# Kernel tuning notes

Measured on AMD Instinct MI355X. Metric: run time of the kernel, lower is better.

## Reference

```python
import jax, jax.numpy as jnp
import numpy as np

NUM_HEADS = 16
HEAD_DIM = 64  # hidden_size 1024 / 16 heads


def setup_inputs() -> dict:
    key = jax.random.key(0)
    ks = jax.random.split(key, 4)
    B, S, H = 2, 2048, 1024
    scale = 1.0 / np.sqrt(H)
    return {
        "hidden_states": jax.random.normal(ks[0], (B, S, H), dtype=jnp.float32),
        "attention_mask": jnp.zeros((B, 1, 1, S), dtype=jnp.float32),
        "Wq": jax.random.normal(ks[1], (H, H), dtype=jnp.float32) * scale,
        "bq": jnp.zeros((H,), dtype=jnp.float32),
        "Wk": jax.random.normal(ks[2], (H, H), dtype=jnp.float32) * scale,
        "bk": jnp.zeros((H,), dtype=jnp.float32),
        "Wv": jax.random.normal(ks[3], (H, H), dtype=jnp.float32) * scale,
        "bv": jnp.zeros((H,), dtype=jnp.float32),
    }


def reference(hidden_states, attention_mask, Wq, bq, Wk, bk, Wv, bv):
    B, S, H = hidden_states.shape
    h, d = NUM_HEADS, HEAD_DIM

    def heads(x):  # [B,S,H] -> [B,h,S,d]
        return x.reshape(B, S, h, d).transpose(0, 2, 1, 3)

    q = heads(hidden_states @ Wq + bq)
    k = heads(hidden_states @ Wk + bk)
    v = heads(hidden_states @ Wv + bv)

    # [B,h,S,S] scores, scaled then additive-masked (HF BERT semantics)
    scores = jnp.einsum("bhqd,bhkd->bhqk", q, k) / jnp.sqrt(jnp.float32(d))
    scores = scores + attention_mask
    probs = jax.nn.softmax(scores, axis=-1)  # dropout p=0 -> identity

    ctx = jnp.einsum("bhqk,bhkd->bhqd", probs, v)
    ctx = ctx.transpose(0, 2, 1, 3).reshape(B, S, H)
    return ctx
```

## Files before the change

kernel.cpp:

```cpp
#include <hip/hip_runtime.h>
#include <hip/hip_bf16.h>


#define SEQ   2048
#define HID   1024
#define NHEAD 16
#define HD    64
#define SD    ((size_t)SEQ * HD)

typedef __bf16 bf16x8 __attribute__((ext_vector_type(8)));
typedef float  f32x4  __attribute__((ext_vector_type(4)));

#define L2E 1.4426950408889634f
#define SOFT_OFF 16.0f

__device__ __forceinline__ unsigned short f2b(float f) {
    unsigned int x = __float_as_uint(f);
    x += 0x7FFFu + ((x >> 16) & 1u);
    return (unsigned short)(x >> 16);
}

__device__ __forceinline__ void gload16(const unsigned short* g,
                                        unsigned short* l) {
    __builtin_amdgcn_global_load_lds(
        (const __attribute__((address_space(1))) unsigned int*)g,
        (__attribute__((address_space(3))) unsigned int*)l, 16, 0, 0);
}

__global__ __launch_bounds__(256) void cvt_x_k(const float* __restrict__ X,
                                               unsigned short* __restrict__ Xb)
{
    const size_t i = ((size_t)blockIdx.x * 256 + threadIdx.x) * 4;
    const float4 v = *(const float4*)(X + i);
    ushort4 o;
    o.x = f2b(v.x); o.y = f2b(v.y); o.z = f2b(v.z); o.w = f2b(v.w);
    *(ushort4*)(Xb + i) = o;
}

__global__ __launch_bounds__(256) void cvt_w_k(
    const float* __restrict__ Wq, const float* __restrict__ Wk,
    const float* __restrict__ Wv, unsigned short* __restrict__ Wtb)
{
    __shared__ __align__(16) unsigned short T[64][68];
    const int z = blockIdx.z;
    const float* __restrict__ W = (z == 0) ? Wq : (z == 1) ? Wk : Wv;
    const int k0 = blockIdx.x * 64, n0 = blockIdx.y * 64;
    const int tid = threadIdx.x;
    #pragma unroll
    for (int it = 0; it < 16; ++it) {
        const int idx = 256 * it + tid;
        const int r = idx >> 6, c = idx & 63;
        T[c][r] = f2b(W[(size_t)(k0 + r) * HID + n0 + c]);
    }
    __syncthreads();
    unsigned short* dst = Wtb + (size_t)z * HID * HID;
    #pragma unroll
    for (int it = 0; it < 4; ++it) {
        const int idx = 256 * it + tid;
        const int n = idx >> 4, c4 = (idx & 15) * 4;
        *(ushort4*)(dst + (size_t)(n0 + n) * HID + k0 + c4) = *(ushort4*)&T[n][c4];
    }
}

__device__ __forceinline__ void gemm_epilogue(
    f32x4 acc[4][4], const float* __restrict__ Bp,
    unsigned short* __restrict__ scratch, unsigned short (*Et)[68],
    int z, int m0, int n0, int wr, int wc, int ln, int quad)
{
    const int b = m0 >> 11;
    const int srow0 = (m0 + wr) & (SEQ - 1);
    const int head = (n0 + wc) >> 6;
    __syncthreads();

    if (z == 2) {
        #pragma unroll
        for (int half = 0; half < 2; ++half) {
            #pragma unroll
            for (int nt2 = 0; nt2 < 2; ++nt2) {
                const int nt = half * 2 + nt2;
                const float bias = Bp[n0 + wc + nt * 16 + ln];
                #pragma unroll
                for (int mt = 0; mt < 4; ++mt) {
                    ushort4 o;
                    o.x = f2b(acc[mt][nt][0] + bias);
                    o.y = f2b(acc[mt][nt][1] + bias);
                    o.z = f2b(acc[mt][nt][2] + bias);
                    o.w = f2b(acc[mt][nt][3] + bias);
                    *(ushort4*)&Et[nt2 * 16 + ln][mt * 16 + quad * 4] = o;
                }
            }
            __syncthreads();
            #pragma unroll
            for (int it = 0; it < 8; ++it) {
                const int d = it * 4 + quad, s4 = ln * 4;
                *(ushort4*)(scratch +
                    ((size_t)(64 + b * NHEAD + head) * HD + half * 32 + d) * SEQ
                    + srow0 + s4) = *(const ushort4*)&Et[d][s4];
            }
            __syncthreads();
        }
    } else {
        #pragma unroll
        for (int half = 0; half < 2; ++half) {
            #pragma unroll
            for (int mt2 = 0; mt2 < 2; ++mt2) {
                const int mt = half * 2 + mt2;
                #pragma unroll
                for (int nt = 0; nt < 4; ++nt) {
                    const float bias = Bp[n0 + wc + nt * 16 + ln];
                    #pragma unroll
                    for (int r = 0; r < 4; ++r)
                        Et[mt2 * 16 + quad * 4 + r][nt * 16 + ln] =
                            f2b(acc[mt][nt][r] + bias);
                }
            }
            __syncthreads();
            #pragma unroll
            for (int it = 0; it < 8; ++it) {
                const int r = it * 4 + quad, c4 = ln * 4;
                *(ushort4*)(scratch +
                    ((size_t)(z * 32 + b * NHEAD + head) * SEQ + srow0
                     + half * 32 + r) * HD + c4) = *(const ushort4*)&Et[r][c4];
            }
            __syncthreads();
        }
    }
}

__global__ __launch_bounds__(256) void qkv_gemm_bf16(
    const unsigned short* __restrict__ Xb, const unsigned short* __restrict__ Wtb,
    const float* __restrict__ bq, const float* __restrict__ bk,
    const float* __restrict__ bv, unsigned short* __restrict__ scratch)
{
    __shared__ __align__(16) unsigned short pool[2][2][128][32];

    const int z = blockIdx.z;
    const float* __restrict__ Bp = (z == 0) ? bq : (z == 1) ? bk : bv;
    const unsigned short* __restrict__ Wz = Wtb + (size_t)z * HID * HID;

    const int tid = threadIdx.x, w = tid >> 6, lane = tid & 63;
    const int ln = lane & 15, quad = lane >> 4;
    const int wr = (w >> 1) * 64, wc = (w & 1) * 64;
    const int m0 = blockIdx.x * 128, n0 = blockIdx.y * 128;

    const int L0 = w * 128 + lane;
    const int r0 = L0 >> 2,        c0 = (L0 & 3) * 8;
    const int r1 = (L0 + 64) >> 2, c1 = ((L0 + 64) & 3) * 8;

    f32x4 acc[4][4];
    #pragma unroll
    for (int i = 0; i < 4; ++i)
        #pragma unroll
        for (int j = 0; j < 4; ++j) acc[i][j] = (f32x4){0.f, 0.f, 0.f, 0.f};

    {
        unsigned short* lx = &pool[0][0][0][0] + (size_t)(w * 128) * 8;
        unsigned short* lw = &pool[0][1][0][0] + (size_t)(w * 128) * 8;
        gload16(Xb + (size_t)(m0 + r0) * HID + c0, lx);
        gload16(Xb + (size_t)(m0 + r1) * HID + c1, lx + 64 * 8);
        gload16(Wz + (size_t)(n0 + r0) * HID + c0, lw);
        gload16(Wz + (size_t)(n0 + r1) * HID + c1, lw + 64 * 8);
    }

    int cur = 0;
    for (int k0 = 0; k0 < HID; k0 += 32) {
        __syncthreads();
        if (k0 + 32 < HID) {
            const int kn = k0 + 32, nxt = cur ^ 1;
            unsigned short* lx = &pool[nxt][0][0][0] + (size_t)(w * 128) * 8;
            unsigned short* lw = &pool[nxt][1][0][0] + (size_t)(w * 128) * 8;
            gload16(Xb + (size_t)(m0 + r0) * HID + kn + c0, lx);
            gload16(Xb + (size_t)(m0 + r1) * HID + kn + c1, lx + 64 * 8);
            gload16(Wz + (size_t)(n0 + r0) * HID + kn + c0, lw);
            gload16(Wz + (size_t)(n0 + r1) * HID + kn + c1, lw + 64 * 8);
        }

        bf16x8 am[4], bn[4];
        #pragma unroll
        for (int t = 0; t < 4; ++t) {
            am[t] = *(const bf16x8*)&pool[cur][0][wr + t * 16 + ln][quad * 8];
            bn[t] = *(const bf16x8*)&pool[cur][1][wc + t * 16 + ln][quad * 8];
        }
        #pragma unroll
        for (int mt = 0; mt < 4; ++mt)
            #pragma unroll
            for (int nt = 0; nt < 4; ++nt)
                acc[mt][nt] = __builtin_amdgcn_mfma_f32_16x16x32_bf16(
                    am[mt], bn[nt], acc[mt][nt], 0, 0, 0);
        cur ^= 1;
    }
    unsigned short (*Et)[68] =
        (unsigned short (*)[68])((unsigned char*)pool + (size_t)w * 4352);
    gemm_epilogue(acc, Bp, scratch, Et, z, m0, n0, wr, wc, ln, quad);
}

__global__ __launch_bounds__(256) void qkv_gemm_fp32(
    const float* __restrict__ X,
    const float* __restrict__ Wq, const float* __restrict__ bq,
    const float* __restrict__ Wk, const float* __restrict__ bk,
    const float* __restrict__ Wv, const float* __restrict__ bv,
    unsigned short* __restrict__ scratch)
{
    __shared__ __align__(16) unsigned char pool[20480];
    unsigned short (*Xs)[40] = (unsigned short (*)[40])pool;
    unsigned short (*Wt)[40] = (unsigned short (*)[40])(pool + 10240);

    const int z = blockIdx.z;
    const float* __restrict__ W  = (z == 0) ? Wq : (z == 1) ? Wk : Wv;
    const float* __restrict__ Bp = (z == 0) ? bq : (z == 1) ? bk : bv;

    const int tid = threadIdx.x, w = tid >> 6, lane = tid & 63;
    const int ln = lane & 15, quad = lane >> 4;
    const int wr = (w >> 1) * 64, wc = (w & 1) * 64;
    const int m0 = blockIdx.x * 128, n0 = blockIdx.y * 128;

    const int xr = tid >> 3, xc = (tid & 7) * 4;
    const int wkr = tid >> 5, wnc = (tid & 31) * 4;

    f32x4 acc[4][4];
    #pragma unroll
    for (int i = 0; i < 4; ++i)
        #pragma unroll
        for (int j = 0; j < 4; ++j) acc[i][j] = (f32x4){0.f, 0.f, 0.f, 0.f};

    for (int k0 = 0; k0 < HID; k0 += 32) {
        __syncthreads();
        #pragma unroll
        for (int it = 0; it < 4; ++it) {
            const int r = xr + 32 * it;
            const float4 xv = *(const float4*)(X + (size_t)(m0 + r) * HID + k0 + xc);
            ushort4 xb;
            xb.x = f2b(xv.x); xb.y = f2b(xv.y); xb.z = f2b(xv.z); xb.w = f2b(xv.w);
            *(ushort4*)&Xs[r][xc] = xb;
            const int kr = wkr + 8 * it;
            const float4 wv = *(const float4*)(W + (size_t)(k0 + kr) * HID + n0 + wnc);
            Wt[wnc + 0][kr] = f2b(wv.x);
            Wt[wnc + 1][kr] = f2b(wv.y);
            Wt[wnc + 2][kr] = f2b(wv.z);
            Wt[wnc + 3][kr] = f2b(wv.w);
        }
        __syncthreads();
        bf16x8 am[4], bn[4];
        #pragma unroll
        for (int t = 0; t < 4; ++t) {
            am[t] = *(const bf16x8*)&Xs[wr + t * 16 + ln][quad * 8];
            bn[t] = *(const bf16x8*)&Wt[wc + t * 16 + ln][quad * 8];
        }
        #pragma unroll
        for (int mt = 0; mt < 4; ++mt)
            #pragma unroll
            for (int nt = 0; nt < 4; ++nt)
                acc[mt][nt] = __builtin_amdgcn_mfma_f32_16x16x32_bf16(
                    am[mt], bn[nt], acc[mt][nt], 0, 0, 0);
    }
    unsigned short (*Et)[68] = (unsigned short (*)[68])(pool + (size_t)w * 4352);
    gemm_epilogue(acc, Bp, scratch, Et, z, m0, n0, wr, wc, ln, quad);
}

__global__ __launch_bounds__(256) void attn_mfma(
    const unsigned short* __restrict__ scratch,
    const float* __restrict__ mask,
    float* __restrict__ out)
{
    __shared__ __align__(16) unsigned char smem[46080];
    unsigned short (*Ks)[64][72] = (unsigned short (*)[64][72])smem;
    unsigned short (*Vt)[64][72] = (unsigned short (*)[64][72])(smem + 18432);
    unsigned short (*Ps)[72]     = (unsigned short (*)[72])(smem + 36864);
    float (*Obuf)[68] = (float (*)[68])smem;

    const int orig = blockIdx.x;
    const int wg = ((orig & 7) << 7) + (orig >> 3);
    const int qt = wg & 31;
    const int bh = wg >> 5;
    const int b = bh >> 4, head = bh & 15;

    const unsigned short* __restrict__ Qp  = scratch + (size_t)bh * SD;
    const unsigned short* __restrict__ Kp  = scratch + (size_t)(32 + bh) * SD;
    const unsigned short* __restrict__ Vtp = scratch + (size_t)(64 + bh) * SD;
    const float* __restrict__ maskp = mask + b * SEQ;

    const int tid = threadIdx.x, w = tid >> 6, lane = tid & 63;
    const int ln = lane & 15, quad = lane >> 4;

    const int qrow = qt * 64 + w * 16 + ln;
    const bf16x8 qb0 = *(const bf16x8*)(Qp + (size_t)qrow * HD + quad * 8);
    const bf16x8 qb1 = *(const bf16x8*)(Qp + (size_t)qrow * HD + 32 + quad * 8);

    f32x4 O[4];
    #pragma unroll
    for (int t = 0; t < 4; ++t) O[t] = (f32x4){0.f, 0.f, 0.f, 0.f};
    float lr = 0.0f;

    const int sr8 = tid >> 3, sc8 = (tid & 7) * 8;

    {
        uint4 a = *(const uint4*)(Kp + (size_t)sr8 * HD + sc8);
        uint4 c = *(const uint4*)(Kp + (size_t)(sr8 + 32) * HD + sc8);
        uint4 d = *(const uint4*)(Vtp + (size_t)sr8 * SEQ + sc8);
        uint4 e = *(const uint4*)(Vtp + (size_t)(sr8 + 32) * SEQ + sc8);
        *(uint4*)&Ks[0][sr8][sc8]      = a;
        *(uint4*)&Ks[0][sr8 + 32][sc8] = c;
        *(uint4*)&Vt[0][sr8][sc8]      = d;
        *(uint4*)&Vt[0][sr8 + 32][sc8] = e;
    }
    uint4 kg0 = *(const uint4*)(Kp + (size_t)(64 + sr8) * HD + sc8);
    uint4 kg1 = *(const uint4*)(Kp + (size_t)(64 + sr8 + 32) * HD + sc8);
    uint4 vg0 = *(const uint4*)(Vtp + (size_t)sr8 * SEQ + 64 + sc8);
    uint4 vg1 = *(const uint4*)(Vtp + (size_t)(sr8 + 32) * SEQ + 64 + sc8);
    __syncthreads();

    for (int kt = 0; kt < 32; ++kt) {
        const int cur = kt & 1;
        if (kt < 31) {
            *(uint4*)&Ks[cur ^ 1][sr8][sc8]      = kg0;
            *(uint4*)&Ks[cur ^ 1][sr8 + 32][sc8] = kg1;
            *(uint4*)&Vt[cur ^ 1][sr8][sc8]      = vg0;
            *(uint4*)&Vt[cur ^ 1][sr8 + 32][sc8] = vg1;
        }
        if (kt < 30) {
            const int kn = kt + 2;
            kg0 = *(const uint4*)(Kp + (size_t)(kn * 64 + sr8) * HD + sc8);
            kg1 = *(const uint4*)(Kp + (size_t)(kn * 64 + sr8 + 32) * HD + sc8);
            vg0 = *(const uint4*)(Vtp + (size_t)sr8 * SEQ + kn * 64 + sc8);
            vg1 = *(const uint4*)(Vtp + (size_t)(sr8 + 32) * SEQ + kn * 64 + sc8);
        }

        f32x4 s[4];
        #pragma unroll
        for (int t = 0; t < 4; ++t) {
            const bf16x8 ka0 = *(const bf16x8*)&Ks[cur][t * 16 + ln][quad * 8];
            const bf16x8 ka1 = *(const bf16x8*)&Ks[cur][t * 16 + ln][32 + quad * 8];
            f32x4 a = (f32x4){0.f, 0.f, 0.f, 0.f};
            a = __builtin_amdgcn_mfma_f32_16x16x32_bf16(ka0, qb0, a, 0, 0, 0);
            a = __builtin_amdgcn_mfma_f32_16x16x32_bf16(ka1, qb1, a, 0, 0, 0);
            s[t] = a;
        }

        const float c = 0.125f * L2E;
        #pragma unroll
        for (int t = 0; t < 4; ++t) {
            const float4 mk4 = *(const float4*)(maskp + kt * 64 + t * 16 + quad * 4);
            const float b0 = fmaf(mk4.x, L2E, -SOFT_OFF);
            const float b1 = fmaf(mk4.y, L2E, -SOFT_OFF);
            const float b2 = fmaf(mk4.z, L2E, -SOFT_OFF);
            const float b3 = fmaf(mk4.w, L2E, -SOFT_OFF);
            const float p0 = exp2f(fmaf(s[t][0], c, b0));
            const float p1 = exp2f(fmaf(s[t][1], c, b1));
            const float p2 = exp2f(fmaf(s[t][2], c, b2));
            const float p3 = exp2f(fmaf(s[t][3], c, b3));
            lr += (p0 + p1) + (p2 + p3);
            unsigned int w0, w1;
            asm("v_cvt_pk_bf16_f32 %0, %1, %2" : "=v"(w0) : "v"(p0), "v"(p1));
            asm("v_cvt_pk_bf16_f32 %0, %1, %2" : "=v"(w1) : "v"(p2), "v"(p3));
            uint2 pw; pw.x = w0; pw.y = w1;
            *(uint2*)&Ps[w * 16 + ln][t * 16 + quad * 4] = pw;
        }

        const bf16x8 pb0 = *(const bf16x8*)&Ps[w * 16 + ln][quad * 8];
        const bf16x8 pb1 = *(const bf16x8*)&Ps[w * 16 + ln][32 + quad * 8];
        #pragma unroll
        for (int t = 0; t < 4; ++t) {
            const bf16x8 va0 = *(const bf16x8*)&Vt[cur][t * 16 + ln][quad * 8];
            const bf16x8 va1 = *(const bf16x8*)&Vt[cur][t * 16 + ln][32 + quad * 8];
            O[t] = __builtin_amdgcn_mfma_f32_16x16x32_bf16(va0, pb0, O[t], 0, 0, 0);
            O[t] = __builtin_amdgcn_mfma_f32_16x16x32_bf16(va1, pb1, O[t], 0, 0, 0);
        }

        __syncthreads();
    }

    lr += __shfl_xor(lr, 16);
    lr += __shfl_xor(lr, 32);

    const float inv = 1.0f / lr;
    #pragma unroll
    for (int t = 0; t < 4; ++t) {
        float4 o4;
        o4.x = O[t][0] * inv; o4.y = O[t][1] * inv;
        o4.z = O[t][2] * inv; o4.w = O[t][3] * inv;
        *(float4*)&Obuf[w * 16 + ln][t * 16 + quad * 4] = o4;
    }
    __syncthreads();
    #pragma unroll
    for (int it = 0; it < 4; ++it) {
        const int r = (tid >> 4) + 16 * it, c4 = (tid & 15) * 4;
        *(float4*)(out + ((size_t)b * SEQ + qt * 64 + r) * HID + head * HD + c4)
            = *(const float4*)&Obuf[r][c4];
    }
}

extern "C" void kernel_launch(void* const* d_in, const int* in_sizes, int n_in,
                              void* d_out, int out_size, void* d_ws, size_t ws_size,
                              hipStream_t stream) {
    const float* X    = (const float*)d_in[0];
    const float* mask = (const float*)d_in[1];
    const float* Wq   = (const float*)d_in[2];
    const float* bq   = (const float*)d_in[3];
    const float* Wk   = (const float*)d_in[4];
    const float* bk   = (const float*)d_in[5];
    const float* Wv   = (const float*)d_in[6];
    const float* bv   = (const float*)d_in[7];

    unsigned short* scratch = (unsigned short*)d_ws;
    float* out = (float*)d_out;

    const bool big = (ws_size >= (40ull << 20));
    if (big) {
        unsigned short* Xb  = scratch + 96 * SD;
        unsigned short* Wtb = Xb + (size_t)2 * SEQ * HID;
        cvt_x_k<<<4096, 256, 0, stream>>>(X, Xb);
        cvt_w_k<<<dim3(16, 16, 3), 256, 0, stream>>>(Wq, Wk, Wv, Wtb);
        qkv_gemm_bf16<<<dim3(32, 8, 3), 256, 0, stream>>>(
            Xb, Wtb, bq, bk, bv, scratch);
    } else {
        qkv_gemm_fp32<<<dim3(32, 8, 3), 256, 0, stream>>>(
            X, Wq, bq, Wk, bk, Wv, bv, scratch);
    }
    attn_mfma<<<1024, 256, 0, stream>>>(scratch, mask, out);
}
```

Baseline: 199.9 us.

## Load K and V fragments directly from global memory instead of LDS staging

The attention kernel no longer stages K and V tiles into double-buffered shared memory. Each wave now reads its MFMA operand fragments straight from global memory (L2-cached), which removes the per-iteration __syncthreads and shrinks LDS use to hold only the P and output buffers. The intent is to cut synchronisation and LDS traffic and to raise occupancy. The cost is that each of the four waves loads the same K/V data separately, which quadruples global/L2 traffic, and the explicit register prefetch of the next tile is lost.

```diff
diff --git a/kernel.cpp b/kernel.cpp
--- a/kernel.cpp
+++ b/kernel.cpp
@@ -262,10 +262,8 @@
     const float* __restrict__ mask,
     float* __restrict__ out)
 {
-    __shared__ __align__(16) unsigned char smem[46080];
-    unsigned short (*Ks)[64][72] = (unsigned short (*)[64][72])smem;
-    unsigned short (*Vt)[64][72] = (unsigned short (*)[64][72])(smem + 18432);
-    unsigned short (*Ps)[72]     = (unsigned short (*)[72])(smem + 36864);
+    __shared__ __align__(16) unsigned char smem[17408];
+    unsigned short (*Ps)[72] = (unsigned short (*)[72])smem;
     float (*Obuf)[68] = (float (*)[68])smem;
 
     const int orig = blockIdx.x;
@@ -291,52 +289,32 @@
     for (int t = 0; t < 4; ++t) O[t] = (f32x4){0.f, 0.f, 0.f, 0.f};
     float lr = 0.0f;
 
-    const int sr8 = tid >> 3, sc8 = (tid & 7) * 8;
-
-    {
-        uint4 a = *(const uint4*)(Kp + (size_t)sr8 * HD + sc8);
-        uint4 c = *(const uint4*)(Kp + (size_t)(sr8 + 32) * HD + sc8);
-        uint4 d = *(const uint4*)(Vtp + (size_t)sr8 * SEQ + sc8);
-        uint4 e = *(const uint4*)(Vtp + (size_t)(sr8 + 32) * SEQ + sc8);
-        *(uint4*)&Ks[0][sr8][sc8]      = a;
-        *(uint4*)&Ks[0][sr8 + 32][sc8] = c;
-        *(uint4*)&Vt[0][sr8][sc8]      = d;
-        *(uint4*)&Vt[0][sr8 + 32][sc8] = e;
-    }
-    uint4 kg0 = *(const uint4*)(Kp + (size_t)(64 + sr8) * HD + sc8);
-    uint4 kg1 = *(const uint4*)(Kp + (size_t)(64 + sr8 + 32) * HD + sc8);
-    uint4 vg0 = *(const uint4*)(Vtp + (size_t)sr8 * SEQ + 64 + sc8);
-    uint4 vg1 = *(const uint4*)(Vtp + (size_t)(sr8 + 32) * SEQ + 64 + sc8);
-    __syncthreads();
+    const float cc = 0.125f * L2E;
 
     for (int kt = 0; kt < 32; ++kt) {
-        const int cur = kt & 1;
-        if (kt < 31) {
-            *(uint4*)&Ks[cur ^ 1][sr8][sc8]      = kg0;
-            *(uint4*)&Ks[cur ^ 1][sr8 + 32][sc8] = kg1;
-            *(uint4*)&Vt[cur ^ 1][sr8][sc8]      = vg0;
-            *(uint4*)&Vt[cur ^ 1][sr8 + 32][sc8] = vg1;
-        }
-        if (kt < 30) {
-            const int kn = kt + 2;
-            kg0 = *(const uint4*)(Kp + (size_t)(kn * 64 + sr8) * HD + sc8);
-            kg1 = *(const uint4*)(Kp + (size_t)(kn * 64 + sr8 + 32) * HD + sc8);
-            vg0 = *(const uint4*)(Vtp + (size_t)sr8 * SEQ + kn * 64 + sc8);
-            vg1 = *(const uint4*)(Vtp + (size_t)(sr8 + 32) * SEQ + kn * 64 + sc8);
+        const unsigned short* kb = Kp + (size_t)kt * 64 * HD;
+        const unsigned short* vb = Vtp + (size_t)kt * 64;
+        bf16x8 kf0[4], kf1[4], vf0[4], vf1[4];
+        #pragma unroll
+        for (int t = 0; t < 4; ++t) {
+            kf0[t] = *(const bf16x8*)(kb + (size_t)(t * 16 + ln) * HD + quad * 8);
+            kf1[t] = *(const bf16x8*)(kb + (size_t)(t * 16 + ln) * HD + 32 + quad * 8);
+        }
+        #pragma unroll
+        for (int t = 0; t < 4; ++t) {
+            vf0[t] = *(const bf16x8*)(vb + (size_t)(t * 16 + ln) * SEQ + quad * 8);
+            vf1[t] = *(const bf16x8*)(vb + (size_t)(t * 16 + ln) * SEQ + 32 + quad * 8);
         }
 
         f32x4 s[4];
         #pragma unroll
         for (int t = 0; t < 4; ++t) {
-            const bf16x8 ka0 = *(const bf16x8*)&Ks[cur][t * 16 + ln][quad * 8];
-            const bf16x8 ka1 = *(const bf16x8*)&Ks[cur][t * 16 + ln][32 + quad * 8];
             f32x4 a = (f32x4){0.f, 0.f, 0.f, 0.f};
-            a = __builtin_amdgcn_mfma_f32_16x16x32_bf16(ka0, qb0, a, 0, 0, 0);
-            a = __builtin_amdgcn_mfma_f32_16x16x32_bf16(ka1, qb1, a, 0, 0, 0);
+            a = __builtin_amdgcn_mfma_f32_16x16x32_bf16(kf0[t], qb0, a, 0, 0, 0);
+            a = __builtin_amdgcn_mfma_f32_16x16x32_bf16(kf1[t], qb1, a, 0, 0, 0);
             s[t] = a;
         }
 
-        const float c = 0.125f * L2E;
         #pragma unroll
         for (int t = 0; t < 4; ++t) {
             const float4 mk4 = *(const float4*)(maskp + kt * 64 + t * 16 + quad * 4);
@@ -344,10 +322,10 @@
             const float b1 = fmaf(mk4.y, L2E, -SOFT_OFF);
             const float b2 = fmaf(mk4.z, L2E, -SOFT_OFF);
             const float b3 = fmaf(mk4.w, L2E, -SOFT_OFF);
-            const float p0 = exp2f(fmaf(s[t][0], c, b0));
-            const float p1 = exp2f(fmaf(s[t][1], c, b1));
-            const float p2 = exp2f(fmaf(s[t][2], c, b2));
-            const float p3 = exp2f(fmaf(s[t][3], c, b3));
+            const float p0 = exp2f(fmaf(s[t][0], cc, b0));
+            const float p1 = exp2f(fmaf(s[t][1], cc, b1));
+            const float p2 = exp2f(fmaf(s[t][2], cc, b2));
+            const float p3 = exp2f(fmaf(s[t][3], cc, b3));
             lr += (p0 + p1) + (p2 + p3);
             unsigned int w0, w1;
             asm("v_cvt_pk_bf16_f32 %0, %1, %2" : "=v"(w0) : "v"(p0), "v"(p1));
@@ -360,18 +338,15 @@
         const bf16x8 pb1 = *(const bf16x8*)&Ps[w * 16 + ln][32 + quad * 8];
         #pragma unroll
         for (int t = 0; t < 4; ++t) {
-            const bf16x8 va0 = *(const bf16x8*)&Vt[cur][t * 16 + ln][quad * 8];
-            const bf16x8 va1 = *(const bf16x8*)&Vt[cur][t * 16 + ln][32 + quad * 8];
-            O[t] = __builtin_amdgcn_mfma_f32_16x16x32_bf16(va0, pb0, O[t], 0, 0, 0);
-            O[t] = __builtin_amdgcn_mfma_f32_16x16x32_bf16(va1, pb1, O[t], 0, 0, 0);
-        }
-
-        __syncthreads();
+            O[t] = __builtin_amdgcn_mfma_f32_16x16x32_bf16(vf0[t], pb0, O[t], 0, 0, 0);
+            O[t] = __builtin_amdgcn_mfma_f32_16x16x32_bf16(vf1[t], pb1, O[t], 0, 0, 0);
+        }
     }
 
     lr += __shfl_xor(lr, 16);
     lr += __shfl_xor(lr, 32);
 
+    __syncthreads();
     const float inv = 1.0f / lr;
     #pragma unroll
     for (int t = 0; t < 4; ++t) {
```

After: 362.5 us. +81.3%, slower.

## Split attention key tiles across waves and reduce partial outputs in LDS

Applied to the files above, without the earlier changes.

Each wave now computes scores for a 16-key slice against all 64 queries of the tile, instead of all 64 keys for its own 16 queries. The goal is to keep the probabilities in registers and drop the shared-memory round-trip for P. The PV product uses zero-padded half-empty MFMA operands, and each wave holds a four-times-larger output accumulator. At the end the partial outputs and row sums from the four waves are combined through LDS with extra barriers. The trade is more MFMA issue, higher register pressure and a cross-wave reduction, in exchange for one fewer LDS store and load per tile and a smaller shared-memory footprint.

```diff
diff --git a/kernel.cpp b/kernel.cpp
--- a/kernel.cpp
+++ b/kernel.cpp
@@ -262,11 +262,12 @@
     const float* __restrict__ mask,
     float* __restrict__ out)
 {
-    __shared__ __align__(16) unsigned char smem[46080];
+    __shared__ __align__(16) unsigned char smem[37888];
     unsigned short (*Ks)[64][72] = (unsigned short (*)[64][72])smem;
     unsigned short (*Vt)[64][72] = (unsigned short (*)[64][72])(smem + 18432);
-    unsigned short (*Ps)[72]     = (unsigned short (*)[72])(smem + 36864);
-    float (*Obuf)[68] = (float (*)[68])smem;
+    float* lrbuf = (float*)(smem + 36864);
+    float (*OA)[68] = (float (*)[68])smem;
+    float (*OB)[68] = (float (*)[68])(smem + 18432);
 
     const int orig = blockIdx.x;
     const int wg = ((orig & 7) << 7) + (orig >> 3);
@@ -281,15 +282,22 @@
 
     const int tid = threadIdx.x, w = tid >> 6, lane = tid & 63;
     const int ln = lane & 15, quad = lane >> 4;
-
-    const int qrow = qt * 64 + w * 16 + ln;
-    const bf16x8 qb0 = *(const bf16x8*)(Qp + (size_t)qrow * HD + quad * 8);
-    const bf16x8 qb1 = *(const bf16x8*)(Qp + (size_t)qrow * HD + 32 + quad * 8);
-
-    f32x4 O[4];
-    #pragma unroll
-    for (int t = 0; t < 4; ++t) O[t] = (f32x4){0.f, 0.f, 0.f, 0.f};
-    float lr = 0.0f;
+    const int wk0 = w * 16;
+
+    bf16x8 qb[4][2];
+    #pragma unroll
+    for (int t = 0; t < 4; ++t)
+        #pragma unroll
+        for (int h = 0; h < 2; ++h)
+            qb[t][h] = *(const bf16x8*)(Qp +
+                (size_t)(qt * 64 + t * 16 + ln) * HD + h * 32 + quad * 8);
+
+    f32x4 O[4][4];
+    #pragma unroll
+    for (int i = 0; i < 4; ++i)
+        #pragma unroll
+        for (int j = 0; j < 4; ++j) O[i][j] = (f32x4){0.f, 0.f, 0.f, 0.f};
+    float lr[4] = {0.f, 0.f, 0.f, 0.f};
 
     const int sr8 = tid >> 3, sc8 = (tid & 7) * 8;
 
@@ -309,6 +317,8 @@
     uint4 vg1 = *(const uint4*)(Vtp + (size_t)(sr8 + 32) * SEQ + 64 + sc8);
     __syncthreads();
 
+    const float cc = 0.125f * L2E;
+
     for (int kt = 0; kt < 32; ++kt) {
         const int cur = kt & 1;
         if (kt < 31) {
@@ -325,68 +335,101 @@
             vg1 = *(const uint4*)(Vtp + (size_t)(sr8 + 32) * SEQ + kn * 64 + sc8);
         }
 
+        const bf16x8 ka0 = *(const bf16x8*)&Ks[cur][wk0 + ln][quad * 8];
+        const bf16x8 ka1 = *(const bf16x8*)&Ks[cur][wk0 + ln][32 + quad * 8];
+
+        uint2 vl[4];
+        #pragma unroll
+        for (int dg = 0; dg < 4; ++dg)
+            vl[dg] = *(const uint2*)&Vt[cur][dg * 16 + ln][wk0 + quad * 4];
+
         f32x4 s[4];
         #pragma unroll
         for (int t = 0; t < 4; ++t) {
-            const bf16x8 ka0 = *(const bf16x8*)&Ks[cur][t * 16 + ln][quad * 8];
-            const bf16x8 ka1 = *(const bf16x8*)&Ks[cur][t * 16 + ln][32 + quad * 8];
             f32x4 a = (f32x4){0.f, 0.f, 0.f, 0.f};
-            a = __builtin_amdgcn_mfma_f32_16x16x32_bf16(ka0, qb0, a, 0, 0, 0);
-            a = __builtin_amdgcn_mfma_f32_16x16x32_bf16(ka1, qb1, a, 0, 0, 0);
+            a = __builtin_amdgcn_mfma_f32_16x16x32_bf16(ka0, qb[t][0], a, 0, 0, 0);
+            a = __builtin_amdgcn_mfma_f32_16x16x32_bf16(ka1, qb[t][1], a, 0, 0, 0);
             s[t] = a;
         }
 
-        const float c = 0.125f * L2E;
+        const float4 mk4 = *(const float4*)(maskp + kt * 64 + wk0 + quad * 4);
+        const float b0 = fmaf(mk4.x, L2E, -SOFT_OFF);
+        const float b1 = fmaf(mk4.y, L2E, -SOFT_OFF);
+        const float b2 = fmaf(mk4.z, L2E, -SOFT_OFF);
+        const float b3 = fmaf(mk4.w, L2E, -SOFT_OFF);
+
+        bf16x8 pb[4];
         #pragma unroll
         for (int t = 0; t < 4; ++t) {
-            const float4 mk4 = *(const float4*)(maskp + kt * 64 + t * 16 + quad * 4);
-            const float b0 = fmaf(mk4.x, L2E, -SOFT_OFF);
-            const float b1 = fmaf(mk4.y, L2E, -SOFT_OFF);
-            const float b2 = fmaf(mk4.z, L2E, -SOFT_OFF);
-            const float b3 = fmaf(mk4.w, L2E, -SOFT_OFF);
-            const float p0 = exp2f(fmaf(s[t][0], c, b0));
-            const float p1 = exp2f(fmaf(s[t][1], c, b1));
-            const float p2 = exp2f(fmaf(s[t][2], c, b2));
-            const float p3 = exp2f(fmaf(s[t][3], c, b3));
-            lr += (p0 + p1) + (p2 + p3);
+            const float p0 = exp2f(fmaf(s[t][0], cc, b0));
+            const float p1 = exp2f(fmaf(s[t][1], cc, b1));
+            const float p2 = exp2f(fmaf(s[t][2], cc, b2));
+            const float p3 = exp2f(fmaf(s[t][3], cc, b3));
+            lr[t] += (p0 + p1) + (p2 + p3);
             unsigned int w0, w1;
             asm("v_cvt_pk_bf16_f32 %0, %1, %2" : "=v"(w0) : "v"(p0), "v"(p1));
             asm("v_cvt_pk_bf16_f32 %0, %1, %2" : "=v"(w1) : "v"(p2), "v"(p3));
-            uint2 pw; pw.x = w0; pw.y = w1;
-            *(uint2*)&Ps[w * 16 + ln][t * 16 + quad * 4] = pw;
-        }
-
-        const bf16x8 pb0 = *(const bf16x8*)&Ps[w * 16 + ln][quad * 8];
-        const bf16x8 pb1 = *(const bf16x8*)&Ps[w * 16 + ln][32 + quad * 8];
-        #pragma unroll
-        for (int t = 0; t < 4; ++t) {
-            const bf16x8 va0 = *(const bf16x8*)&Vt[cur][t * 16 + ln][quad * 8];
-            const bf16x8 va1 = *(const bf16x8*)&Vt[cur][t * 16 + ln][32 + quad * 8];
-            O[t] = __builtin_amdgcn_mfma_f32_16x16x32_bf16(va0, pb0, O[t], 0, 0, 0);
-            O[t] = __builtin_amdgcn_mfma_f32_16x16x32_bf16(va1, pb1, O[t], 0, 0, 0);
+            uint4 pu; pu.x = w0; pu.y = w1; pu.z = w0; pu.w = w1;
+            pb[t] = *(bf16x8*)&pu;
+        }
+
+        #pragma unroll
+        for (int dg = 0; dg < 4; ++dg) {
+            uint4 vu; vu.x = vl[dg].x; vu.y = vl[dg].y; vu.z = 0u; vu.w = 0u;
+            const bf16x8 va = *(bf16x8*)&vu;
+            #pragma unroll
+            for (int t = 0; t < 4; ++t)
+                O[dg][t] = __builtin_amdgcn_mfma_f32_16x16x32_bf16(
+                    va, pb[t], O[dg][t], 0, 0, 0);
         }
 
         __syncthreads();
     }
 
-    lr += __shfl_xor(lr, 16);
-    lr += __shfl_xor(lr, 32);
-
-    const float inv = 1.0f / lr;
     #pragma unroll
     for (int t = 0; t < 4; ++t) {
-        float4 o4;
-        o4.x = O[t][0] * inv; o4.y = O[t][1] * inv;
-        o4.z = O[t][2] * inv; o4.w = O[t][3] * inv;
-        *(float4*)&Obuf[w * 16 + ln][t * 16 + quad * 4] = o4;
-    }
-    __syncthreads();
+        lr[t] += __shfl_xor(lr[t], 16);
+        lr[t] += __shfl_xor(lr[t], 32);
+    }
+    if (quad == 0) {
+        #pragma unroll
+        for (int t = 0; t < 4; ++t) lrbuf[w * 64 + t * 16 + ln] = lr[t];
+    }
+
+    #define O_WRITE(BUF) { \
+        _Pragma("unroll") for (int dg = 0; dg < 4; ++dg) \
+        _Pragma("unroll") for (int t = 0; t < 4; ++t) \
+            *(float4*)&BUF[t * 16 + ln][dg * 16 + quad * 4] = \
+                *(float4*)&O[dg][t]; }
+    #define O_ADD(BUF) { \
+        _Pragma("unroll") for (int dg = 0; dg < 4; ++dg) \
+        _Pragma("unroll") for (int t = 0; t < 4; ++t) { \
+            const float4 x = *(const float4*)&BUF[t * 16 + ln][dg * 16 + quad * 4]; \
+            O[dg][t][0] += x.x; O[dg][t][1] += x.y; \
+            O[dg][t][2] += x.z; O[dg][t][3] += x.w; } }
+
+    if (w == 1) O_WRITE(OA);
+    if (w == 3) O_WRITE(OB);
+    __syncthreads();
+    if (w == 0) O_ADD(OA);
+    if (w == 2) O_ADD(OB);
+    __syncthreads();
+    if (w == 2) O_WRITE(OA);
+    __syncthreads();
+    if (w == 0) { O_ADD(OA); O_WRITE(OA); }
+    __syncthreads();
+
     #pragma unroll
     for (int it = 0; it < 4; ++it) {
         const int r = (tid >> 4) + 16 * it, c4 = (tid & 15) * 4;
-        *(float4*)(out + ((size_t)b * SEQ + qt * 64 + r) * HID + head * HD + c4)
-            = *(const float4*)&Obuf[r][c4];
-    }
+        const float lrt = lrbuf[r] + lrbuf[64 + r] + lrbuf[128 + r] + lrbuf[192 + r];
+        const float inv = 1.0f / lrt;
+        float4 v = *(const float4*)&OA[r][c4];
+        v.x *= inv; v.y *= inv; v.z *= inv; v.w *= inv;
+        *(float4*)(out + ((size_t)b * SEQ + qt * 64 + r) * HID + head * HD + c4) = v;
+    }
+    #undef O_WRITE
+    #undef O_ADD
 }
 
 extern "C" void kernel_launch(void* const* d_in, const int* in_sizes, int n_in,
```

After: 204.5 us. 1.02x slower.
